# Performance work log

Hardware: AMD Instinct MI355X
Metric: run time of the kernel (lower is better)

The kernel has to match this reference:

```python
import jax, jax.numpy as jnp
import numpy as np

HIDDEN = 2048
N_HEADS = 16
HEAD_DIM = HIDDEN // N_HEADS
MAX_POS = 4096
ROPE_THETA = 10000.0
B, S = 2, 4096


def rotate_half(x):
    d = x.shape[-1] // 2
    return jnp.concatenate([-x[..., d:], x[..., :d]], axis=-1)


def make_rope_cache(seq_len, dim, base):
    inv_freq = 1.0 / (base ** (np.arange(0, dim, 2, dtype=np.float32) / dim))
    t = np.arange(seq_len, dtype=np.float32)
    freqs = np.einsum('i,j->ij', t, inv_freq)
    emb = np.concatenate([freqs, freqs], axis=-1)
    return jnp.asarray(np.cos(emb)), jnp.asarray(np.sin(emb))


def setup_inputs() -> dict:
    key = jax.random.key(0)
    k1, k2, k3, k4, k5, k6 = jax.random.split(key, 6)
    hidden_states = jax.random.normal(k1, (B, S, HIDDEN), dtype=jnp.float32)
    # causal additive mask [B,1,S,S]
    causal = jnp.where(jnp.tril(jnp.ones((S, S), dtype=bool)), 0.0, -1e9).astype(jnp.float32)
    attention_mask = jnp.broadcast_to(causal[None, None], (B, 1, S, S))
    position_ids = jnp.broadcast_to(jnp.arange(S, dtype=jnp.int64)[None], (B, S))
    scale = 0.02
    Wq = jax.random.normal(k2, (HIDDEN, HIDDEN), dtype=jnp.float32) * scale
    Wk = jax.random.normal(k3, (HIDDEN, HIDDEN), dtype=jnp.float32) * scale
    Wv = jax.random.normal(k4, (HIDDEN, HIDDEN), dtype=jnp.float32) * scale
    Wo = jax.random.normal(k5, (HIDDEN, HIDDEN), dtype=jnp.float32) * scale
    return {"hidden_states": hidden_states, "attention_mask": attention_mask,
            "position_ids": position_ids, "Wq": Wq, "Wk": Wk, "Wv": Wv, "Wo": Wo}


def reference(hidden_states, attention_mask, position_ids, Wq, Wk, Wv, Wo):
    bsz, q_len, _ = hidden_states.shape
    # projections (torch Linear: x @ W.T; here W stored as [in,out] -> x @ W)
    q = (hidden_states @ Wq).reshape(bsz, q_len, N_HEADS, HEAD_DIM).transpose(0, 2, 1, 3)
    k = (hidden_states @ Wk).reshape(bsz, q_len, N_HEADS, HEAD_DIM).transpose(0, 2, 1, 3)
    v = (hidden_states @ Wv).reshape(bsz, q_len, N_HEADS, HEAD_DIM).transpose(0, 2, 1, 3)
    cos_c, sin_c = make_rope_cache(q_len, HEAD_DIM, ROPE_THETA)
    cos = cos_c[position_ids][:, None]  # [B,1,S,Dh]
    sin = sin_c[position_ids][:, None]
    q = q * cos + rotate_half(q) * sin
    k = k * cos + rotate_half(k) * sin
    scores = jnp.einsum('bhqd,bhkd->bhqk', q, k) / jnp.sqrt(jnp.float32(HEAD_DIM))
    scores = scores + attention_mask
    probs = jax.nn.softmax(scores.astype(jnp.float32), axis=-1).astype(q.dtype)
    attn = jnp.einsum('bhqk,bhkd->bhqd', probs, v)
    attn = attn.transpose(0, 2, 1, 3).reshape(bsz, q_len, HIDDEN)
    return attn @ Wo
```

## Files before the change

### kernel.cpp

```cpp
#include <hip/hip_runtime.h>

#define HID 2048
#define NHEADS 16
#define DHEAD 128
#define BB 2
#define SS 4096
#define MTOT (BB * SS)

typedef __attribute__((ext_vector_type(8))) short short8;
typedef __attribute__((ext_vector_type(8))) unsigned short ushort8;
typedef __attribute__((ext_vector_type(4))) float floatx4;
typedef __attribute__((ext_vector_type(16))) float floatx16;

static __device__ __forceinline__ ushort f2bf(float f) {
  unsigned x = __float_as_uint(f);
  return (ushort)((x + 0x7fffu + ((x >> 16) & 1u)) >> 16);
}
static __device__ __forceinline__ float bf2f(ushort u) {
  return __uint_as_float(((unsigned)u) << 16);
}
static __device__ __forceinline__ unsigned cvtpk_bf16(float lo, float hi) {
  unsigned r;
  asm("v_cvt_pk_bf16_f32 %0, %1, %2" : "=v"(r) : "v"(lo), "v"(hi));
  return r;
}
static __device__ __forceinline__ void pl32swap(unsigned& a, unsigned& b) {
  asm volatile("v_permlane32_swap_b32 %0, %1" : "+v"(a), "+v"(b));
}
static __device__ __forceinline__ floatx16 fz16() {
  floatx16 z;
#pragma unroll
  for (int i = 0; i < 16; i++) z[i] = 0.f;
  return z;
}

#define GL16(g, l)                                                   \
  __builtin_amdgcn_global_load_lds(                                  \
      (const __attribute__((address_space(1))) unsigned int*)(g),    \
      (__attribute__((address_space(3))) unsigned int*)(l), 16, 0, 0)

__global__ __launch_bounds__(256) void k_prep(const float* __restrict__ X,
                                              ushort* __restrict__ Xb,
                                              const float* __restrict__ Wq,
                                              const float* __restrict__ Wk,
                                              const float* __restrict__ Wv,
                                              const float* __restrict__ Wo,
                                              ushort* __restrict__ Wqt,
                                              ushort* __restrict__ Wkt,
                                              ushort* __restrict__ Wvt,
                                              ushort* __restrict__ Wot,
                                              float* __restrict__ cosT,
                                              float* __restrict__ sinT) {
  __shared__ float tile[64][65];
  int id = blockIdx.x, t = threadIdx.x;
  if (id < 2048) {
    int i = id * 256 + t;
    const int n4 = MTOT * HID / 4, stride = 2048 * 256;
    for (; i < n4; i += stride) {
      float4 v = reinterpret_cast<const float4*>(X)[i];
      ushort4 u;
      u.x = f2bf(v.x); u.y = f2bf(v.y); u.z = f2bf(v.z); u.w = f2bf(v.w);
      reinterpret_cast<ushort4*>(Xb)[i] = u;
    }
  } else if (id < 6144) {
    int w = (id - 2048) >> 10;
    int bid = (id - 2048) & 1023;
    const float* W = (w == 0) ? Wq : (w == 1) ? Wk : (w == 2) ? Wv : Wo;
    ushort* Wt = (w == 0) ? Wqt : (w == 1) ? Wkt : (w == 2) ? Wvt : Wot;
    int n0 = (bid & 31) * 64, k0 = (bid >> 5) * 64;
#pragma unroll
    for (int i = 0; i < 16; i++) {
      int idx = t + i * 256, r = idx >> 6, c = idx & 63;
      tile[r][c] = W[(size_t)(k0 + r) * HID + n0 + c];
    }
    __syncthreads();
#pragma unroll
    for (int i = 0; i < 16; i++) {
      int idx = t + i * 256, r = idx >> 6, c = idx & 63;
      Wt[(size_t)(n0 + r) * HID + k0 + c] = f2bf(tile[c][r]);
    }
  } else {
    int idx = (id - 6144) * 256 + t;
    int pos = idx >> 6, j = idx & 63;
    float inv = powf(10000.0f, -(float)(2 * j) * (1.0f / 128.0f));
    float a = (float)pos * inv;
    cosT[idx] = cosf(a);
    sinT[idx] = sinf(a);
  }
}

__global__ void k_rope(ushort* __restrict__ Q, ushort* __restrict__ Kb,
                       const float* __restrict__ cosT, const float* __restrict__ sinT) {
  const float kSc = 0.12751742f;
  int idx = blockIdx.x * 256 + threadIdx.x;
  int j8 = (idx & 7) * 8;
  int hh = (idx >> 3) & (NHEADS - 1);
  int srow = idx >> 7;
  int pos = srow & (SS - 1);
  float4 c0 = *reinterpret_cast<const float4*>(&cosT[pos * 64 + j8]);
  float4 c1 = *reinterpret_cast<const float4*>(&cosT[pos * 64 + j8 + 4]);
  float4 s0 = *reinterpret_cast<const float4*>(&sinT[pos * 64 + j8]);
  float4 s1 = *reinterpret_cast<const float4*>(&sinT[pos * 64 + j8 + 4]);
  float cc[8] = {c0.x, c0.y, c0.z, c0.w, c1.x, c1.y, c1.z, c1.w};
  float ss[8] = {s0.x, s0.y, s0.z, s0.w, s1.x, s1.y, s1.z, s1.w};
  size_t base = (size_t)srow * HID + hh * DHEAD + j8;
  ushort8 qa = *reinterpret_cast<ushort8*>(&Q[base]);
  ushort8 qb = *reinterpret_cast<ushort8*>(&Q[base + 64]);
  ushort8 ka = *reinterpret_cast<ushort8*>(&Kb[base]);
  ushort8 kb = *reinterpret_cast<ushort8*>(&Kb[base + 64]);
  ushort8 o1, o2, o3, o4;
#pragma unroll
  for (int i = 0; i < 8; i++) {
    float a1 = bf2f(qa[i]), a2 = bf2f(qb[i]);
    o1[i] = f2bf((a1 * cc[i] - a2 * ss[i]) * kSc);
    o2[i] = f2bf((a2 * cc[i] + a1 * ss[i]) * kSc);
    float b1 = bf2f(ka[i]), b2 = bf2f(kb[i]);
    o3[i] = f2bf(b1 * cc[i] - b2 * ss[i]);
    o4[i] = f2bf(b2 * cc[i] + b1 * ss[i]);
  }
  *reinterpret_cast<ushort8*>(&Q[base]) = o1;
  *reinterpret_cast<ushort8*>(&Q[base + 64]) = o2;
  *reinterpret_cast<ushort8*>(&Kb[base]) = o3;
  *reinterpret_cast<ushort8*>(&Kb[base + 64]) = o4;
}

template <int OUT_BF16, int DUAL>
__global__ __launch_bounds__(512, 2) void k_gemm8(const ushort* __restrict__ A,
                                                  const ushort* __restrict__ Bt,
                                                  void* __restrict__ Cp,
                                                  const ushort* __restrict__ Bt2,
                                                  void* __restrict__ Cp2,
                                                  int Mr, int Nc, int Kd) {
  __shared__ ushort As[3][256 * 32];
  __shared__ ushort Bs[3][256 * 32];
  int t = threadIdx.x;
  int lane = t & 63, wid = t >> 6;
  int lrow = lane & 15, lk = lane >> 4;
  int wr = wid >> 2, wc = wid & 3;

  int id = blockIdx.x;
  if (DUAL && id >= 256) {
    Bt = Bt2;
    Cp = Cp2;
    id -= 256;
  }
  int nbx = Nc >> 8;
  int swz = (id & 7) * 32 + (id >> 3);
  int m0 = (swz / nbx) << 8, n0 = (swz % nbx) << 8;

  floatx4 acc[8][4];
#pragma unroll
  for (int i = 0; i < 8; i++)
#pragma unroll
    for (int j = 0; j < 4; j++) acc[i][j] = (floatx4){0.f, 0.f, 0.f, 0.f};

  int arow = t >> 2;
  int acol = (((t & 3) ^ (arow & 3)) << 3);
  const ushort* gA = A + (size_t)(m0 + arow) * Kd + acol;
  const ushort* gB = Bt + (size_t)(n0 + arow) * Kd + acol;

  auto STAGE = [&](int buf, int kt) {
    const ushort* a = gA + kt * 32;
    const ushort* bq = gB + kt * 32;
    GL16(a, (char*)As + buf * 16384 + t * 16);
    GL16(a + (size_t)128 * Kd, (char*)As + buf * 16384 + t * 16 + 8192);
    GL16(bq, (char*)Bs + buf * 16384 + t * 16);
    GL16(bq + (size_t)128 * Kd, (char*)Bs + buf * 16384 + t * 16 + 8192);
  };

  STAGE(0, 0);
  STAGE(1, 1);

  int nk = Kd >> 5;
  for (int tK = 0; tK < nk; ++tK) {
    if (tK + 1 < nk)
      asm volatile("s_waitcnt vmcnt(4)" ::: "memory");
    else
      asm volatile("s_waitcnt vmcnt(0)" ::: "memory");
    __builtin_amdgcn_s_barrier();
    asm volatile("" ::: "memory");
    int buf = tK % 3;
    const char* Ab_ = (const char*)As + buf * 16384;
    const char* Bb_ = (const char*)Bs + buf * 16384;
    short8 af[8], bfr[4];
#pragma unroll
    for (int fm = 0; fm < 8; fm++) {
      int row = wr * 128 + fm * 16 + lrow;
      af[fm] = *reinterpret_cast<const short8*>(
          Ab_ + ((row * 64 + lk * 16) ^ ((row & 3) << 4)));
    }
#pragma unroll
    for (int fn = 0; fn < 4; fn++) {
      int row = wc * 64 + fn * 16 + lrow;
      bfr[fn] = *reinterpret_cast<const short8*>(
          Bb_ + ((row * 64 + lk * 16) ^ ((row & 3) << 4)));
    }
    if (tK + 2 < nk) STAGE((tK + 2) % 3, tK + 2);
    __builtin_amdgcn_s_setprio(1);
#pragma unroll
    for (int fm = 0; fm < 8; fm++)
#pragma unroll
      for (int fn = 0; fn < 4; fn++)
        acc[fm][fn] = __builtin_amdgcn_mfma_f32_16x16x32_bf16(af[fm], bfr[fn],
                                                              acc[fm][fn], 0, 0, 0);
    __builtin_amdgcn_s_setprio(0);
  }

#pragma unroll
  for (int am = 0; am < 8; am++)
#pragma unroll
    for (int an = 0; an < 4; an++)
#pragma unroll
      for (int r = 0; r < 4; r++) {
        int m = m0 + wr * 128 + am * 16 + lk * 4 + r;
        int n = n0 + wc * 64 + an * 16 + lrow;
        if (OUT_BF16)
          ((ushort*)Cp)[(size_t)m * Nc + n] = f2bf(acc[am][an][r]);
        else
          ((float*)Cp)[(size_t)m * Nc + n] = acc[am][an][r];
      }
}

__global__ __launch_bounds__(512, 2) void k_fattn(const ushort* __restrict__ Qg,
                                                  const ushort* __restrict__ Kg,
                                                  const ushort* __restrict__ Vt2,
                                                  ushort* __restrict__ Og) {
  __shared__ ushort Ks[2][64 * 128];
  __shared__ ushort Vs[2][128 * 64];
  int t = threadIdx.x, lane = t & 63, wid = t >> 6;
  int l31 = lane & 31, hi = lane >> 5;
  int id = blockIdx.x;
  int qt = 15 - (id >> 5);
  int h = id & 15, b = (id >> 4) & 1;

  auto STAGE = [&](int buf, int kt) {
    int kv0 = kt * 64;
    const ushort* Kbase = Kg + (size_t)(b * SS + kv0) * HID + h * DHEAD;
    const ushort* Vbase = Vt2 + (size_t)(h * DHEAD) * MTOT + b * SS + kv0;
#pragma unroll
    for (int i = 0; i < 2; i++) {
      int L = t + i * 512;
      int row = L >> 4, cr = L & 15;
      GL16(Kbase + (size_t)row * HID + ((cr ^ (row & 15)) << 3),
           (char*)Ks + buf * 16384 + L * 16);
    }
#pragma unroll
    for (int i = 0; i < 2; i++) {
      int L = t + i * 512;
      int row = L >> 3, cr = L & 7;
      GL16(Vbase + (size_t)row * MTOT + ((cr ^ (row & 7)) << 3),
           (char*)Vs + buf * 16384 + L * 16);
    }
  };

  int q0 = qt * 256;
  int wq0 = q0 + wid * 32;
  int qlane = wq0 + l31;

  short8 qf[8];
  {
    const ushort* qb = Qg + (size_t)(b * SS + qlane) * HID + h * DHEAD + hi * 8;
#pragma unroll
    for (int ks = 0; ks < 8; ks++)
      qf[ks] = *reinterpret_cast<const short8*>(qb + ks * 16);
  }

  floatx16 accO[4];
#pragma unroll
  for (int db = 0; db < 4; db++) accO[db] = fz16();
  float mrow = -1e30f, lsum = 0.f;

  int nkt = (qt + 1) * 4;
  STAGE(0, 0);

  for (int kt = 0; kt < nkt; kt++) {
    int cur = kt & 1;
    int kv0 = kt * 64;
    bool pre = (kt + 1 < nkt);
    if (pre) {
      STAGE(cur ^ 1, kt + 1);
      asm volatile("s_waitcnt vmcnt(4)" ::: "memory");
    } else {
      asm volatile("s_waitcnt vmcnt(0)" ::: "memory");
    }
    __builtin_amdgcn_s_barrier();
    asm volatile("" ::: "memory");

    if (kv0 <= wq0 + 31) {
      const char* Kb_ = (const char*)Ks + cur * 16384;
      floatx16 accS[2];
      accS[0] = fz16(); accS[1] = fz16();
      __builtin_amdgcn_s_setprio(1);
#pragma unroll
      for (int ks = 0; ks < 8; ks++) {
#pragma unroll
        for (int kvb = 0; kvb < 2; kvb++) {
          int row = kvb * 32 + l31;
          int byte_ = (row * 256 + ks * 32 + hi * 16) ^ ((row & 15) << 4);
          short8 kf = *reinterpret_cast<const short8*>(Kb_ + byte_);
          accS[kvb] = __builtin_amdgcn_mfma_f32_32x32x16_bf16(kf, qf[ks], accS[kvb], 0, 0, 0);
        }
      }
      __builtin_amdgcn_s_setprio(0);

      if (kv0 + 63 > wq0) {
        int kvbase = kv0 + hi * 4;
#pragma unroll
        for (int kvb = 0; kvb < 2; kvb++)
#pragma unroll
          for (int r = 0; r < 16; r++) {
            int kvi = kvbase + kvb * 32 + (r & 3) + 8 * (r >> 2);
            if (kvi > qlane) accS[kvb][r] = -1e30f;
          }
      }

      float mA = -1e30f, mB = -1e30f, mC = -1e30f, mD = -1e30f;
#pragma unroll
      for (int r = 0; r < 16; r += 4) {
        mA = fmaxf(mA, fmaxf(accS[0][r], accS[1][r]));
        mB = fmaxf(mB, fmaxf(accS[0][r + 1], accS[1][r + 1]));
        mC = fmaxf(mC, fmaxf(accS[0][r + 2], accS[1][r + 2]));
        mD = fmaxf(mD, fmaxf(accS[0][r + 3], accS[1][r + 3]));
      }
      float mx = fmaxf(fmaxf(mA, mB), fmaxf(mC, mD));
      mx = fmaxf(mx, __shfl_xor(mx, 32));
      if (!__all(mx <= mrow + 8.0f)) {
        float mnew = fmaxf(mrow, mx);
        float corr = exp2f(mrow - mnew);
        mrow = mnew;
        lsum *= corr;
#pragma unroll
        for (int db = 0; db < 4; db++)
#pragma unroll
          for (int r = 0; r < 16; r++) accO[db][r] *= corr;
      }

      float sA = 0.f, sB = 0.f, sC = 0.f, sD = 0.f;
#pragma unroll
      for (int kvb = 0; kvb < 2; kvb++)
#pragma unroll
        for (int r = 0; r < 16; r += 4) {
          float p0 = exp2f(accS[kvb][r] - mrow);
          float p1 = exp2f(accS[kvb][r + 1] - mrow);
          float p2 = exp2f(accS[kvb][r + 2] - mrow);
          float p3 = exp2f(accS[kvb][r + 3] - mrow);
          accS[kvb][r] = p0; accS[kvb][r + 1] = p1;
          accS[kvb][r + 2] = p2; accS[kvb][r + 3] = p3;
          sA += p0; sB += p1; sC += p2; sD += p3;
        }
      lsum += ((sA + sB) + (sC + sD));

      const char* Vb_ = (const char*)Vs + cur * 16384;
#pragma unroll
      for (int ks = 0; ks < 4; ks++) {
        int kvb = ks >> 1, tt = ks & 1;
        unsigned w0 = cvtpk_bf16(accS[kvb][8 * tt + 0], accS[kvb][8 * tt + 1]);
        unsigned w2 = cvtpk_bf16(accS[kvb][8 * tt + 4], accS[kvb][8 * tt + 5]);
        pl32swap(w0, w2);
        unsigned w1 = cvtpk_bf16(accS[kvb][8 * tt + 2], accS[kvb][8 * tt + 3]);
        unsigned w3 = cvtpk_bf16(accS[kvb][8 * tt + 6], accS[kvb][8 * tt + 7]);
        pl32swap(w1, w3);
        union { unsigned u[4]; short8 v; } pf;
        pf.u[0] = w0; pf.u[1] = w1; pf.u[2] = w2; pf.u[3] = w3;
        __builtin_amdgcn_s_setprio(1);
#pragma unroll
        for (int db = 0; db < 4; db++) {
          int row = db * 32 + l31;
          int byte_ = (row * 128 + ks * 32 + hi * 16) ^ ((row & 7) << 4);
          short8 vf = *reinterpret_cast<const short8*>(Vb_ + byte_);
          accO[db] = __builtin_amdgcn_mfma_f32_32x32x16_bf16(vf, pf.v, accO[db], 0, 0, 0);
        }
        __builtin_amdgcn_s_setprio(0);
      }
    }
    asm volatile("" ::: "memory");
    __builtin_amdgcn_s_barrier();
    asm volatile("" ::: "memory");
  }

  float lt = lsum + __shfl_xor(lsum, 32);
  float inv = 1.0f / lt;
  char* sb = ((wid < 4) ? (char*)Ks : (char*)Vs) + (wid & 3) * 8192;
#pragma unroll
  for (int db = 0; db < 4; db++)
#pragma unroll
    for (int r = 0; r < 16; r += 2) {
      int d = db * 32 + (r & 3) + 8 * (r >> 2) + hi * 4;
      unsigned w = cvtpk_bf16(accO[db][r] * inv, accO[db][r + 1] * inv);
      int byte_ = (l31 * 256 + d * 2) ^ ((l31 & 15) << 4);
      *reinterpret_cast<unsigned*>(sb + byte_) = w;
    }
#pragma unroll
  for (int i = 0; i < 8; i++) {
    int row = i * 4 + (lane >> 4);
    int byte_ = (row * 256 + (lane & 15) * 16) ^ ((row & 15) << 4);
    ushort8 ov = *reinterpret_cast<const ushort8*>(sb + byte_);
    *reinterpret_cast<ushort8*>(Og + (size_t)(b * SS + wq0 + row) * HID + h * DHEAD +
                                (lane & 15) * 8) = ov;
  }
}

extern "C" void kernel_launch(void* const* d_in, const int* in_sizes, int n_in,
                              void* d_out, int out_size, void* d_ws, size_t ws_size,
                              hipStream_t stream) {
  const float* X = (const float*)d_in[0];
  const float* Wq = (const float*)d_in[3];
  const float* Wk = (const float*)d_in[4];
  const float* Wv = (const float*)d_in[5];
  const float* Wo = (const float*)d_in[6];
  float* out = (float*)d_out;

  char* p = (char*)d_ws;
  const size_t szXb = (size_t)MTOT * HID * 2;
  const size_t szW = (size_t)HID * HID * 2;
  ushort* Xb = (ushort*)p;  p += szXb;
  ushort* Wqt = (ushort*)p; p += szW;
  ushort* Wkt = (ushort*)p; p += szW;
  ushort* Wvt = (ushort*)p; p += szW;
  ushort* Wot = (ushort*)p; p += szW;
  ushort* Qb = (ushort*)p;  p += szXb;
  ushort* Kb = (ushort*)p;  p += szXb;
  ushort* Vt2 = (ushort*)p; p += szXb;
  ushort* Ab = (ushort*)p;  p += szXb;
  float* cosT = (float*)p;  p += (size_t)SS * 64 * 4;
  float* sinT = (float*)p;  p += (size_t)SS * 64 * 4;

  k_prep<<<7168, 256, 0, stream>>>(X, Xb, Wq, Wk, Wv, Wo, Wqt, Wkt, Wvt, Wot,
                                   cosT, sinT);

  k_gemm8<1, 1><<<512, 512, 0, stream>>>(Xb, Wqt, Qb, Wkt, Kb, MTOT, HID, HID);
  k_gemm8<1, 0><<<256, 512, 0, stream>>>(Wvt, Xb, Vt2, nullptr, nullptr, HID, MTOT, HID);

  k_rope<<<MTOT * NHEADS * 8 / 256, 256, 0, stream>>>(Qb, Kb, cosT, sinT);

  k_fattn<<<512, 512, 0, stream>>>(Qb, Kb, Vt2, Ab);

  k_gemm8<0, 0><<<256, 512, 0, stream>>>(Ab, Wot, out, nullptr, nullptr, MTOT, HID, HID);
}
```

Measured before the change: 518.4 us.

## Merge Q/K/V projection GEMMs into one launch and use raw v_exp_f32 in attention

Folds the V-transposed projection into the dual Q/K GEMM launch as a third block range, so one 768-block launch covers all three projections and the separate V launch with its tail is gone. The flash-attention softmax swaps exp2f for the raw v_exp_f32 instruction, which skips the range and denormal handling that exp2f adds. The rope kernel moves to 512-thread blocks. The exp change can give different results for very negative inputs, though masked scores there are already tiny.

```diff
diff --git a/kernel.cpp b/kernel.cpp
--- a/kernel.cpp
+++ b/kernel.cpp
@@ -26,6 +26,11 @@
 }
 static __device__ __forceinline__ void pl32swap(unsigned& a, unsigned& b) {
   asm volatile("v_permlane32_swap_b32 %0, %1" : "+v"(a), "+v"(b));
+}
+static __device__ __forceinline__ float exp2_fast(float x) {
+  float r;
+  asm("v_exp_f32 %0, %1" : "=v"(r) : "v"(x));
+  return r;
 }
 static __device__ __forceinline__ floatx16 fz16() {
   floatx16 z;
@@ -89,10 +94,12 @@
   }
 }
 
-__global__ void k_rope(ushort* __restrict__ Q, ushort* __restrict__ Kb,
-                       const float* __restrict__ cosT, const float* __restrict__ sinT) {
+__global__ __launch_bounds__(512) void k_rope(ushort* __restrict__ Q,
+                                              ushort* __restrict__ Kb,
+                                              const float* __restrict__ cosT,
+                                              const float* __restrict__ sinT) {
   const float kSc = 0.12751742f;
-  int idx = blockIdx.x * 256 + threadIdx.x;
+  int idx = blockIdx.x * 512 + threadIdx.x;
   int j8 = (idx & 7) * 8;
   int hh = (idx >> 3) & (NHEADS - 1);
   int srow = idx >> 7;
@@ -124,13 +131,16 @@
   *reinterpret_cast<ushort8*>(&Kb[base + 64]) = o4;
 }
 
-template <int OUT_BF16, int DUAL>
+template <int OUT_BF16, int TRIPLE>
 __global__ __launch_bounds__(512, 2) void k_gemm8(const ushort* __restrict__ A,
                                                   const ushort* __restrict__ Bt,
                                                   void* __restrict__ Cp,
                                                   const ushort* __restrict__ Bt2,
                                                   void* __restrict__ Cp2,
-                                                  int Mr, int Nc, int Kd) {
+                                                  const ushort* __restrict__ A3,
+                                                  const ushort* __restrict__ Bt3,
+                                                  void* __restrict__ Cp3,
+                                                  int Nc0, int Kd) {
   __shared__ ushort As[3][256 * 32];
   __shared__ ushort Bs[3][256 * 32];
   int t = threadIdx.x;
@@ -139,9 +149,12 @@
   int wr = wid >> 2, wc = wid & 3;
 
   int id = blockIdx.x;
-  if (DUAL && id >= 256) {
-    Bt = Bt2;
-    Cp = Cp2;
+  int Nc = Nc0;
+  if (TRIPLE && id >= 512) {
+    A = A3; Bt = Bt3; Cp = Cp3; Nc = MTOT;
+    id -= 512;
+  } else if (TRIPLE && id >= 256) {
+    Bt = Bt2; Cp = Cp2;
     id -= 256;
   }
   int nbx = Nc >> 8;
@@ -326,7 +339,7 @@
       mx = fmaxf(mx, __shfl_xor(mx, 32));
       if (!__all(mx <= mrow + 8.0f)) {
         float mnew = fmaxf(mrow, mx);
-        float corr = exp2f(mrow - mnew);
+        float corr = exp2_fast(mrow - mnew);
         mrow = mnew;
         lsum *= corr;
 #pragma unroll
@@ -340,10 +353,10 @@
       for (int kvb = 0; kvb < 2; kvb++)
 #pragma unroll
         for (int r = 0; r < 16; r += 4) {
-          float p0 = exp2f(accS[kvb][r] - mrow);
-          float p1 = exp2f(accS[kvb][r + 1] - mrow);
-          float p2 = exp2f(accS[kvb][r + 2] - mrow);
-          float p3 = exp2f(accS[kvb][r + 3] - mrow);
+          float p0 = exp2_fast(accS[kvb][r] - mrow);
+          float p1 = exp2_fast(accS[kvb][r + 1] - mrow);
+          float p2 = exp2_fast(accS[kvb][r + 2] - mrow);
+          float p3 = exp2_fast(accS[kvb][r + 3] - mrow);
           accS[kvb][r] = p0; accS[kvb][r + 1] = p1;
           accS[kvb][r + 2] = p2; accS[kvb][r + 3] = p3;
           sA += p0; sB += p1; sC += p2; sD += p3;
@@ -428,12 +441,12 @@
   k_prep<<<7168, 256, 0, stream>>>(X, Xb, Wq, Wk, Wv, Wo, Wqt, Wkt, Wvt, Wot,
                                    cosT, sinT);
 
-  k_gemm8<1, 1><<<512, 512, 0, stream>>>(Xb, Wqt, Qb, Wkt, Kb, MTOT, HID, HID);
-  k_gemm8<1, 0><<<256, 512, 0, stream>>>(Wvt, Xb, Vt2, nullptr, nullptr, HID, MTOT, HID);
-
-  k_rope<<<MTOT * NHEADS * 8 / 256, 256, 0, stream>>>(Qb, Kb, cosT, sinT);
+  k_gemm8<1, 1><<<768, 512, 0, stream>>>(Xb, Wqt, Qb, Wkt, Kb, Wvt, Xb, Vt2,
+                                         HID, HID);
+  k_rope<<<MTOT * NHEADS * 8 / 512, 512, 0, stream>>>(Qb, Kb, cosT, sinT);
 
   k_fattn<<<512, 512, 0, stream>>>(Qb, Kb, Vt2, Ab);
 
-  k_gemm8<0, 0><<<256, 512, 0, stream>>>(Ab, Wot, out, nullptr, nullptr, MTOT, HID, HID);
-}
+  k_gemm8<0, 0><<<256, 512, 0, stream>>>(Ab, Wot, out, nullptr, nullptr,
+                                         nullptr, nullptr, nullptr, HID, HID);
+}
```

New measurement: 488.1 us. 5.8% less time.
